# Optimization experiments

Hardware: AMD Instinct MI355X
Metric: run time of the kernel (lower is better)

## Reference

```python
import jax, jax.numpy as jnp
import numpy as np

SIGMA_V = 0.1   # std of topic-level Gaussian noise theta_V
SCALE_R = 0.1   # 'sigma2_R' is used as the Normal scale in the torch code


def setup_inputs() -> dict:
    key = jax.random.key(0)
    ks = jax.random.split(key, 8)
    T, L, NT, KC, D = 20, 2000, 1000, 256, 5
    return {
        "Q": jax.random.normal(ks[0], (NT, 32), dtype=jnp.float32),
        "V": jax.random.normal(ks[1], (NT, KC), dtype=jnp.float32),
        "R": jax.random.uniform(ks[2], (T, L, NT), dtype=jnp.float32),
        "neighbor_weights": jax.random.normal(ks[3], (NT, NT), dtype=jnp.float32),
        "U": jax.random.normal(ks[4], (T, L, KC, D), dtype=jnp.float32),
        "U_emb_w": jax.random.normal(ks[5], (1, D), dtype=jnp.float32),
        "U_emb_b": jax.random.normal(ks[6], (1,), dtype=jnp.float32),
        "noise": jax.random.normal(ks[7], (NT, KC), dtype=jnp.float32),
        "C": jax.random.randint(jax.random.fold_in(key, 9), (T, L, NT), 0, 2, dtype=jnp.int32),
    }


def reference(Q, V, R, neighbor_weights, U, U_emb_w, U_emb_b, noise, C):
    # (nw[:, :, None] * V[None]).sum(0)[b, k] == V[b, k] * nw.sum(0)[b]
    # -> avoid materializing the (nt, nt, kc) intermediate.
    V_j = V * jnp.sum(neighbor_weights, axis=0)[:, None] + SIGMA_V * noise  # (nt, kc)
    # Linear(dim=5 -> 1) applied to U, then squeeze: (T, L, kc)
    U_emb = jnp.einsum('tlkd,d->tlk', U, U_emb_w[0]) + U_emb_b[0]
    # scores[t, i, j] = sigmoid(U_emb[t, i, :] . V_j[j, :])
    mu = jax.nn.sigmoid(jnp.einsum('tlk,jk->tlj', U_emb, V_j))  # (T, L, nt)
    # Normal(mu, SCALE_R).log_prob(R), summed over entries where C == 1
    log_prob = (-0.5 * jnp.square((R - mu) / SCALE_R)
                - jnp.log(SCALE_R) - 0.5 * jnp.log(2.0 * jnp.pi))
    return jnp.sum(jnp.where(C == 1, log_prob, 0.0))
```

## Files before the change

### kernel.cpp

```cpp
#include <hip/hip_runtime.h>
#include <hip/hip_bf16.h>

typedef __attribute__((ext_vector_type(8))) short short8;
typedef __attribute__((ext_vector_type(4))) float f32x4;
typedef __attribute__((ext_vector_type(4))) int   i32x4;

#define NTOP 1000
#define KC   256
#define MROWS 40000
#define MBLK  64

static __device__ __forceinline__ unsigned short f2bf(float x) {
    union { float f; unsigned u; } v; v.f = x;
    unsigned r = (v.u + 0x7FFFu + ((v.u >> 16) & 1u)) >> 16;
    return (unsigned short)r;
}

__global__ void k_prep(const float* __restrict__ nw,
                       float* __restrict__ colsum) {
    int j  = blockIdx.x * 256 + threadIdx.x;
    int i0 = blockIdx.y * 8;
    if (j < NTOP) {
        float s = 0.f;
        int iend = min(i0 + 8, NTOP);
        for (int i = i0; i < iend; ++i) s += nw[(size_t)i * NTOP + j];
        atomicAdd(colsum + j, s);
    }
}

__global__ void k_vj(const float* __restrict__ V,
                     const float* __restrict__ noise,
                     const float* __restrict__ colsum,
                     unsigned short* __restrict__ Bp) {
    int t  = blockIdx.x * 256 + threadIdx.x;
    int nt = t >> 9;
    int s  = (t >> 6) & 7;
    int l  = t & 63;
    int lm = l & 15, lq = l >> 4;
    int n  = nt * 16 + lm;
    int k0 = s * 32 + lq * 8;
    union { short8 v; unsigned short us[8]; } pk;
    if (n < NTOP) {
        float cs = colsum[n];
        #pragma unroll
        for (int j = 0; j < 8; ++j) {
            int idx = n * KC + k0 + j;
            pk.us[j] = f2bf(V[idx] * cs + 0.1f * noise[idx]);
        }
    } else {
        #pragma unroll
        for (int j = 0; j < 8; ++j) pk.us[j] = 0;
    }
    reinterpret_cast<short8*>(Bp)[t] = pk.v;
}

__global__ __launch_bounds__(256) void k_cmask(const int* __restrict__ C,
                                               unsigned* __restrict__ Cb) {
    const int idx = blockIdx.x * 256 + threadIdx.x;
    const int m = idx >> 5, w = idx & 31;
    const int* p = C + (size_t)m * NTOP + w * 32;
    const int nbase = w * 32;
    unsigned word = 0;
    if (nbase + 32 <= NTOP) {
        #pragma unroll
        for (int j = 0; j < 32; j += 4) {
            i32x4 c4 = *reinterpret_cast<const i32x4*>(p + j);
            word |= (unsigned)(c4.x == 1) << (j + 0);
            word |= (unsigned)(c4.y == 1) << (j + 1);
            word |= (unsigned)(c4.z == 1) << (j + 2);
            word |= (unsigned)(c4.w == 1) << (j + 3);
        }
    } else {
        for (int j = 0; j < NTOP - nbase; ++j)
            word |= (unsigned)(p[j] == 1) << j;
    }
    Cb[idx] = word;
}

__global__ __launch_bounds__(256, 3) void k_main(
    const float* __restrict__ U, const float* __restrict__ w5,
    const float* __restrict__ b1, const short8* __restrict__ Bf,
    const float* __restrict__ R, const unsigned* __restrict__ Cb,
    float* __restrict__ out)
{
    __shared__ short8 Afrag[4][8][64];
    __shared__ float  rawU[5120];

    const int tid  = threadIdx.x;
    const int wave = tid >> 6;
    const int l    = tid & 63;
    const int lm = l & 15;
    const int lq = l >> 4;
    const int m0 = blockIdx.x * MBLK;

    const float w0 = w5[0], w1 = w5[1], w2 = w5[2], w3 = w5[3], w4 = w5[4];
    const float bb = b1[0];

    const float* ub = U + (size_t)m0 * (KC * 5);
    for (int g = 0; g < 16; ++g) {
        const float* src = ub + (size_t)g * 5120;
        #pragma unroll
        for (int j = 0; j < 5; ++j) {
            const int idx = j * 1024 + tid * 4;
            *reinterpret_cast<f32x4*>(&rawU[idx]) =
                *reinterpret_cast<const f32x4*>(src + idx);
        }
        __syncthreads();
        if (tid < 128) {
            const int s   = tid >> 4;
            const int lqc = (tid >> 2) & 3;
            const int lmh = tid & 3;
            const int fi  = lmh * 1280 + s * 160 + lqc * 40;
            float u[40];
            #pragma unroll
            for (int i = 0; i < 10; ++i) {
                f32x4 t = *reinterpret_cast<const f32x4*>(&rawU[fi + i * 4]);
                u[i*4+0] = t.x; u[i*4+1] = t.y; u[i*4+2] = t.z; u[i*4+3] = t.w;
            }
            union { short8 v; unsigned short us[8]; } pk;
            #pragma unroll
            for (int j = 0; j < 8; ++j) {
                float e = u[j*5+0]*w0 + u[j*5+1]*w1 + u[j*5+2]*w2
                        + u[j*5+3]*w3 + u[j*5+4]*w4 + bb;
                pk.us[j] = f2bf(e);
            }
            const int mt = g >> 2;
            const int ll = lqc * 16 + ((g & 3) * 4 + lmh);
            Afrag[mt][s][ll] = pk.v;
        }
        __syncthreads();
    }

    const size_t rb0 = (size_t)(m0 +  0 + lm) * NTOP;
    const size_t rb1 = (size_t)(m0 + 16 + lm) * NTOP;
    const size_t rb2 = (size_t)(m0 + 32 + lm) * NTOP;
    const size_t rb3 = (size_t)(m0 + 48 + lm) * NTOP;
    const size_t cb0 = (size_t)(m0 +  0 + lm) * 32;
    const size_t cb1 = (size_t)(m0 + 16 + lm) * 32;
    const size_t cb2 = (size_t)(m0 + 32 + lm) * 32;
    const size_t cb3 = (size_t)(m0 + 48 + lm) * 32;

    auto LOADIT = [&](int nt16_, f32x4* rv_, unsigned* cw_) {
        const int nst = (nt16_ << 4) + (lq << 2);
        if (nst < NTOP) {
            const int ws = nst >> 5;
            rv_[0] = *reinterpret_cast<const f32x4*>(R + rb0 + nst);
            rv_[1] = *reinterpret_cast<const f32x4*>(R + rb1 + nst);
            rv_[2] = *reinterpret_cast<const f32x4*>(R + rb2 + nst);
            rv_[3] = *reinterpret_cast<const f32x4*>(R + rb3 + nst);
            cw_[0] = Cb[cb0 + ws];
            cw_[1] = Cb[cb1 + ws];
            cw_[2] = Cb[cb2 + ws];
            cw_[3] = Cb[cb3 + ws];
        } else {
            #pragma unroll
            for (int q = 0; q < 4; ++q) {
                rv_[q] = (f32x4){0.f, 0.f, 0.f, 0.f};
                cw_[q] = 0u;
            }
        }
    };

    auto LOADBF = [&](int nt16_, short8* b_) {
        #pragma unroll
        for (int s = 0; s < 8; ++s)
            b_[s] = Bf[((nt16_ * 8 + s) << 6) + l];
    };

    float lpsum = 0.f;
    const int nt0 = wave << 4;

    short8 bfc[8], bfn[8];
    f32x4 rv[4]; unsigned cw[4];
    LOADBF(nt0, bfc);
    LOADIT(nt0, rv, cw);

    for (int it = 0; it < 16; ++it) {
        const int nt16 = nt0 + it;

        __builtin_amdgcn_sched_barrier(0);
        if (it < 15) LOADBF(nt16 + 1, bfn);
        __builtin_amdgcn_sched_barrier(0);

        f32x4 acc[4];
        #pragma unroll
        for (int mt = 0; mt < 4; ++mt) acc[mt] = (f32x4){0.f, 0.f, 0.f, 0.f};

        #pragma unroll
        for (int s = 0; s < 8; ++s) {
            const short8 bfr = bfc[s];
            const short8 a0 = Afrag[0][s][l];
            const short8 a1 = Afrag[1][s][l];
            const short8 a2 = Afrag[2][s][l];
            const short8 a3 = Afrag[3][s][l];
            acc[0] = __builtin_amdgcn_mfma_f32_16x16x32_bf16(bfr, a0, acc[0], 0, 0, 0);
            acc[1] = __builtin_amdgcn_mfma_f32_16x16x32_bf16(bfr, a1, acc[1], 0, 0, 0);
            acc[2] = __builtin_amdgcn_mfma_f32_16x16x32_bf16(bfr, a2, acc[2], 0, 0, 0);
            acc[3] = __builtin_amdgcn_mfma_f32_16x16x32_bf16(bfr, a3, acc[3], 0, 0, 0);
        }

        f32x4 rv2[4]; unsigned cw2[4];

        __builtin_amdgcn_sched_barrier(0);
        if (it < 15) LOADIT(nt16 + 1, rv2, cw2);
        __builtin_amdgcn_sched_barrier(0);

        const int sh = ((nt16 & 1) << 4) + (lq << 2);
        #pragma unroll
        for (int mt = 0; mt < 4; ++mt) {
            const unsigned y = cw[mt] >> sh;
            #pragma unroll
            for (int r = 0; r < 4; ++r) {
                float muv = 1.f / (1.f + __expf(-acc[mt][r]));
                float d   = rv[mt][r] - muv;
                float lp  = -50.f * d * d + 1.3836465597893728f;
                if ((y >> r) & 1u) lpsum += lp;
            }
        }

        if (it < 15) {
            #pragma unroll
            for (int s = 0; s < 8; ++s) bfc[s] = bfn[s];
            rv[0] = rv2[0]; cw[0] = cw2[0];
            rv[1] = rv2[1]; cw[1] = cw2[1];
            rv[2] = rv2[2]; cw[2] = cw2[2];
            rv[3] = rv2[3]; cw[3] = cw2[3];
        }
    }

    #pragma unroll
    for (int off = 32; off > 0; off >>= 1) lpsum += __shfl_down(lpsum, off);
    if (l == 0) atomicAdd(out, lpsum);
}

extern "C" void kernel_launch(void* const* d_in, const int* in_sizes, int n_in,
                              void* d_out, int out_size, void* d_ws, size_t ws_size,
                              hipStream_t stream) {
    const float* V     = (const float*)d_in[1];
    const float* R     = (const float*)d_in[2];
    const float* nw    = (const float*)d_in[3];
    const float* U     = (const float*)d_in[4];
    const float* w5    = (const float*)d_in[5];
    const float* b1    = (const float*)d_in[6];
    const float* noise = (const float*)d_in[7];
    const int*   C     = (const int*)d_in[8];
    float* out = (float*)d_out;

    float*          colsum = (float*)d_ws;
    unsigned short* Bp     = (unsigned short*)((char*)d_ws + 8192);
    unsigned*       Cb     = (unsigned*)((char*)d_ws + 532480);

    hipMemsetAsync(colsum, 0, NTOP * sizeof(float), stream);
    hipMemsetAsync(out, 0, sizeof(float), stream);
    hipLaunchKernelGGL(k_prep, dim3(4, 125), dim3(256), 0, stream, nw, colsum);
    hipLaunchKernelGGL(k_vj, dim3(128), dim3(256), 0, stream,
                       V, noise, colsum, Bp);
    hipLaunchKernelGGL(k_cmask, dim3(5000), dim3(256), 0, stream, C, Cb);
    hipLaunchKernelGGL(k_main, dim3(MROWS / MBLK), dim3(256), 0, stream,
                       U, w5, b1, (const short8*)Bp, R, Cb, out);
}
```

Measured before the change: 176.2 us.

## Prefetch next U chunk into registers and split embedding across all threads

The U staging loop now issues the global loads for chunk g+1 into registers while chunk g is processed from shared memory, so global latency overlaps with compute. All 256 threads now compute the embedding, each handling half of a chunk (4 elements instead of 8). The shared buffer is padded to a row stride of 1284 floats to cut bank conflicts. This adds register pressure from the five f32x4 prefetch registers.

```diff
diff --git a/kernel.cpp b/kernel.cpp
--- a/kernel.cpp
+++ b/kernel.cpp
@@ -4,6 +4,7 @@
 typedef __attribute__((ext_vector_type(8))) short short8;
 typedef __attribute__((ext_vector_type(4))) float f32x4;
 typedef __attribute__((ext_vector_type(4))) int   i32x4;
+typedef __attribute__((ext_vector_type(4))) unsigned short us4;
 
 #define NTOP 1000
 #define KC   256
@@ -84,7 +85,7 @@
     float* __restrict__ out)
 {
     __shared__ short8 Afrag[4][8][64];
-    __shared__ float  rawU[5120];
+    __shared__ float  rawU[4 * 1284];
 
     const int tid  = threadIdx.x;
     const int wave = tid >> 6;
@@ -96,39 +97,69 @@
     const float w0 = w5[0], w1 = w5[1], w2 = w5[2], w3 = w5[3], w4 = w5[4];
     const float bb = b1[0];
 
-    const float* ub = U + (size_t)m0 * (KC * 5);
-    for (int g = 0; g < 16; ++g) {
-        const float* src = ub + (size_t)g * 5120;
-        #pragma unroll
-        for (int j = 0; j < 5; ++j) {
-            const int idx = j * 1024 + tid * 4;
-            *reinterpret_cast<f32x4*>(&rawU[idx]) =
-                *reinterpret_cast<const f32x4*>(src + idx);
-        }
-        __syncthreads();
-        if (tid < 128) {
-            const int s   = tid >> 4;
-            const int lqc = (tid >> 2) & 3;
-            const int lmh = tid & 3;
-            const int fi  = lmh * 1280 + s * 160 + lqc * 40;
-            float u[40];
-            #pragma unroll
-            for (int i = 0; i < 10; ++i) {
-                f32x4 t = *reinterpret_cast<const f32x4*>(&rawU[fi + i * 4]);
-                u[i*4+0] = t.x; u[i*4+1] = t.y; u[i*4+2] = t.z; u[i*4+3] = t.w;
-            }
-            union { short8 v; unsigned short us[8]; } pk;
-            #pragma unroll
-            for (int j = 0; j < 8; ++j) {
-                float e = u[j*5+0]*w0 + u[j*5+1]*w1 + u[j*5+2]*w2
-                        + u[j*5+3]*w3 + u[j*5+4]*w4 + bb;
-                pk.us[j] = f2bf(e);
-            }
-            const int mt = g >> 2;
-            const int ll = lqc * 16 + ((g & 3) * 4 + lmh);
-            Afrag[mt][s][ll] = pk.v;
-        }
-        __syncthreads();
+    {
+        const float* ub = U + (size_t)m0 * (KC * 5);
+
+        float* dst0; float* dst1; float* dst2; float* dst3; float* dst4;
+        {
+            int i0 = 0 * 1024 + tid * 4; dst0 = &rawU[(i0 / 1280) * 1284 + i0 % 1280];
+            int i1 = 1 * 1024 + tid * 4; dst1 = &rawU[(i1 / 1280) * 1284 + i1 % 1280];
+            int i2 = 2 * 1024 + tid * 4; dst2 = &rawU[(i2 / 1280) * 1284 + i2 % 1280];
+            int i3 = 3 * 1024 + tid * 4; dst3 = &rawU[(i3 / 1280) * 1284 + i3 % 1280];
+            int i4 = 4 * 1024 + tid * 4; dst4 = &rawU[(i4 / 1280) * 1284 + i4 % 1280];
+        }
+        const int chunk = tid >> 1;
+        const int half  = tid & 1;
+        const int s_c   = chunk >> 4;
+        const int lqc   = (chunk >> 2) & 3;
+        const int lmh   = chunk & 3;
+        const int fi    = lmh * 1284 + s_c * 160 + lqc * 40 + half * 20;
+
+        f32x4 st0, st1, st2, st3, st4;
+        st0 = *reinterpret_cast<const f32x4*>(ub + 0 * 1024 + tid * 4);
+        st1 = *reinterpret_cast<const f32x4*>(ub + 1 * 1024 + tid * 4);
+        st2 = *reinterpret_cast<const f32x4*>(ub + 2 * 1024 + tid * 4);
+        st3 = *reinterpret_cast<const f32x4*>(ub + 3 * 1024 + tid * 4);
+        st4 = *reinterpret_cast<const f32x4*>(ub + 4 * 1024 + tid * 4);
+
+        for (int g = 0; g < 16; ++g) {
+            *reinterpret_cast<f32x4*>(dst0) = st0;
+            *reinterpret_cast<f32x4*>(dst1) = st1;
+            *reinterpret_cast<f32x4*>(dst2) = st2;
+            *reinterpret_cast<f32x4*>(dst3) = st3;
+            *reinterpret_cast<f32x4*>(dst4) = st4;
+            __syncthreads();
+
+            if (g < 15) {
+                const float* src = ub + (size_t)(g + 1) * 5120;
+                st0 = *reinterpret_cast<const f32x4*>(src + 0 * 1024 + tid * 4);
+                st1 = *reinterpret_cast<const f32x4*>(src + 1 * 1024 + tid * 4);
+                st2 = *reinterpret_cast<const f32x4*>(src + 2 * 1024 + tid * 4);
+                st3 = *reinterpret_cast<const f32x4*>(src + 3 * 1024 + tid * 4);
+                st4 = *reinterpret_cast<const f32x4*>(src + 4 * 1024 + tid * 4);
+            }
+
+            {
+                float u[20];
+                #pragma unroll
+                for (int i = 0; i < 5; ++i) {
+                    f32x4 t = *reinterpret_cast<const f32x4*>(&rawU[fi + i * 4]);
+                    u[i*4+0] = t.x; u[i*4+1] = t.y; u[i*4+2] = t.z; u[i*4+3] = t.w;
+                }
+                us4 pk;
+                #pragma unroll
+                for (int j = 0; j < 4; ++j) {
+                    float e = u[j*5+0]*w0 + u[j*5+1]*w1 + u[j*5+2]*w2
+                            + u[j*5+3]*w3 + u[j*5+4]*w4 + bb;
+                    pk[j] = f2bf(e);
+                }
+                const int mt = g >> 2;
+                const int ll = lqc * 16 + ((g & 3) * 4 + lmh);
+                *reinterpret_cast<us4*>(
+                    reinterpret_cast<unsigned short*>(&Afrag[mt][s_c][ll]) + half * 4) = pk;
+            }
+            __syncthreads();
+        }
     }
 
     const size_t rb0 = (size_t)(m0 +  0 + lm) * NTOP;
```

Result: no change. 175.3 us (-0.5%).
